# Kernel optimization log

Measured on AMD Instinct MI355X. Metric: run time of the kernel, lower is better.

Reference implementation:

```python
import jax, jax.numpy as jnp
import numpy as np

B, T, D, L, VOCAB = 4, 2048, 512, 3, 256


def setup_inputs() -> dict:
    key = jax.random.key(0)
    ks = jax.random.split(key, 5)
    x = jax.random.randint(ks[0], (B, T), 0, VOCAB, dtype=jnp.int32)
    embed = jax.random.normal(ks[1], (VOCAB, D), dtype=jnp.float32) * 0.02
    k = jnp.ones((L,), dtype=jnp.float32)
    ln_gamma = jnp.ones((L, D), dtype=jnp.float32)
    ln_beta = jnp.zeros((L, D), dtype=jnp.float32)
    W1 = jax.random.normal(ks[2], (L, D, 4 * D), dtype=jnp.float32) * 0.02
    b1 = jnp.zeros((L, 4 * D), dtype=jnp.float32)
    W2 = jax.random.normal(ks[3], (L, 4 * D, D), dtype=jnp.float32) * 0.02
    b2 = jnp.zeros((L, D), dtype=jnp.float32)
    return {"x": x, "embed": embed, "k": k, "ln_gamma": ln_gamma,
            "ln_beta": ln_beta, "W1": W1, "b1": b1, "W2": W2, "b2": b2}


def _layernorm(x, g, b, eps=1e-3):  # keras default eps=1e-3
    mu = jnp.mean(x, axis=-1, keepdims=True)
    var = jnp.mean(jnp.square(x - mu), axis=-1, keepdims=True)
    return (x - mu) * jax.lax.rsqrt(var + eps) * g + b


def reference(x, embed, k, ln_gamma, ln_beta, W1, b1, W2, b2):
    h = embed[x]  # (B,T,D)
    # CumprodBoundaryDimension: cumprod over feature dim, tanh, cumsum over time
    bd = jnp.cumsum(jnp.tanh(jnp.cumprod(h, axis=-1)), axis=1)
    h = h + h * bd
    t = jnp.arange(T)
    dist = jnp.abs((t[:, None] - t[None, :]).astype(jnp.float32))  # (T,T)
    causal = (t[None, :] <= t[:, None]).astype(jnp.float32)
    for l in range(L):
        # DeltaImportance
        h_cum = jnp.cumsum(h, axis=1)
        h_prev = jnp.pad(h[:, :-1, :], ((0, 0), (1, 0), (0, 0)))
        mag = jnp.linalg.norm(h_cum - h_prev, axis=-1)  # (B,T)
        decay = jnp.exp(-jax.nn.softplus(k[l]) * dist) * causal  # (T,T)
        # importance[b,i,j] = mag[b,i]*decay[i,j]; context = importance @ h
        ctx = jnp.abs(mag[:, :, None] * jnp.einsum('ij,bjd->bid', decay, h))
        y = _layernorm(ctx, ln_gamma[l], ln_beta[l])
        y = jax.nn.gelu(y @ W1[l] + b1[l], approximate=False) @ W2[l] + b2[l]
        h = h + y
    return h @ embed.T  # tied output projection (B,T,VOCAB)
```

## Files before the change

kernel.cpp:

```cpp
#include <hip/hip_runtime.h>
#include <math.h>


constexpr int Bc = 4, Tc = 2048, Dc = 512, Hc = 2048, Vc = 256;
constexpr int TSF = 16, NCF = 128;

typedef __attribute__((ext_vector_type(8))) short short8;
typedef __attribute__((ext_vector_type(4))) float f32x4;

__device__ inline unsigned short f2bf(float f) {
  unsigned int u = __float_as_uint(f);
  u += 0x7fffu + ((u >> 16) & 1u);
  return (unsigned short)(u >> 16);
}

__device__ inline void gload_lds16(const void* g, void* l) {
  __builtin_amdgcn_global_load_lds(
      (const __attribute__((address_space(1))) void*)g,
      (__attribute__((address_space(3))) void*)l, 16, 0, 0);
}

__device__ inline float gelu_f(float z) {
  float x = z * 0.707106781186547524f;
  float ax = fabsf(x);
  float t = 1.0f / (1.0f + 0.3275911f * ax);
  float poly = t*(0.254829592f + t*(-0.284496736f + t*(1.421413741f +
               t*(-1.453152027f + t*1.061405429f))));
  float er = 1.0f - poly * __expf(-ax*ax);
  er = copysignf(er, x);
  return 0.5f * z * (1.0f + er);
}

__device__ inline float decay_w(const float* kvec, int l) {
  float kk = kvec[l];
  float sp = kk > 0.f ? kk + log1pf(expf(-kk)) : log1pf(expf(kk));
  return expf(-sp);
}

__device__ inline void tr32(const float* Wl, unsigned short* Wtl,
                            int R, int C, int c0, int r0, int tid,
                            float (*tile)[33]) {
  int tx = tid & 31, ty = tid >> 5;
  for (int i = ty; i < 32; i += 8)
    tile[i][tx] = Wl[(size_t)(r0+i)*C + (c0+tx)];
  __syncthreads();
  int rx = tid & 7, ry = tid >> 3;
  ushort4 o;
  o.x = f2bf(tile[rx*4+0][ry]);
  o.y = f2bf(tile[rx*4+1][ry]);
  o.z = f2bf(tile[rx*4+2][ry]);
  o.w = f2bf(tile[rx*4+3][ry]);
  *(ushort4*)&Wtl[(size_t)(c0+ry)*R + (r0 + rx*4)] = o;
}

__global__ __launch_bounds__(256) void wprep(
    const float* __restrict__ W1, unsigned short* __restrict__ W1t,
    const float* __restrict__ W2, unsigned short* __restrict__ W2t,
    const float* __restrict__ embed, unsigned short* __restrict__ emb)
{
  __shared__ float tile[32][33];
  int bid = blockIdx.x, tid = threadIdx.x;
  if (bid < 3072) {
    int l = bid >> 10, rem = bid & 1023;
    int cx = rem & 63, ry = rem >> 6;
    tr32(W1 + (size_t)l*Dc*Hc, W1t + (size_t)l*Dc*Hc, Dc, Hc,
         cx*32, ry*32, tid, tile);
  } else if (bid < 6144) {
    int b2 = bid - 3072;
    int l = b2 >> 10, rem = b2 & 1023;
    int cx = rem & 15, ry = rem >> 4;
    tr32(W2 + (size_t)l*Hc*Dc, W2t + (size_t)l*Hc*Dc, Hc, Dc,
         cx*32, ry*32, tid, tile);
  } else {
    int i = ((bid - 6144)*256 + tid) * 4;
    if (i < Vc*Dc) {
      float4 v = *(const float4*)&embed[i];
      ushort4 o;
      o.x = f2bf(v.x); o.y = f2bf(v.y); o.z = f2bf(v.z); o.w = f2bf(v.w);
      *(ushort4*)&emb[i] = o;
    }
  }
}

__global__ __launch_bounds__(1024) void embed_part(
    const int* __restrict__ x, const float* __restrict__ embed,
    float* __restrict__ th, float* __restrict__ partA)
{
  int c = blockIdx.x, b = blockIdx.y;
  int wv = threadIdx.x >> 6, lane = threadIdx.x & 63;
  int token = b*Tc + c*TSF + wv;
  int row = x[token];
  const float* e = embed + (size_t)row * Dc + lane * 8;
  float v[8];
  {
    float4 a = *(const float4*)e;
    float4 bb = *(const float4*)(e + 4);
    v[0]=a.x; v[1]=a.y; v[2]=a.z; v[3]=a.w;
    v[4]=bb.x; v[5]=bb.y; v[6]=bb.z; v[7]=bb.w;
  }
  float p = v[0];
  #pragma unroll
  for (int j=1;j<8;++j) p *= v[j];
  float incl = p;
  #pragma unroll
  for (int off=1; off<64; off<<=1) {
    float t = __shfl_up(incl, off);
    if (lane >= off) incl *= t;
  }
  float excl = __shfl_up(incl, 1);
  if (lane == 0) excl = 1.0f;
  float cc = excl;
  float o[8];
  #pragma unroll
  for (int j=0;j<8;++j) { cc *= v[j]; o[j] = tanhf(cc); }
  float* dst = th + (size_t)token * Dc + lane * 8;
  *(float4*)dst     = make_float4(o[0],o[1],o[2],o[3]);
  *(float4*)(dst+4) = make_float4(o[4],o[5],o[6],o[7]);
  __syncthreads();
  int d = threadIdx.x;
  if (d < Dc) {
    const float* pp = th + ((size_t)b*Tc + c*TSF)*Dc + d;
    float s = 0.f;
    #pragma unroll
    for (int t=0;t<TSF;++t) s += pp[(size_t)t*Dc];
    partA[((size_t)b*NCF + c)*Dc + d] = s;
  }
}

__global__ __launch_bounds__(512) void part_prefix(float* __restrict__ part)
{
  int pair = blockIdx.x * 8 + (threadIdx.x >> 6);
  int lane = threadIdx.x & 63;
  int b = pair >> 9, d = pair & 511;
  size_t i0 = ((size_t)b*NCF + 2*lane)*Dc + d;
  float v0 = part[i0];
  float v1 = part[i0 + Dc];
  float ps = v0 + v1;
  float incl = ps;
  #pragma unroll
  for (int off=1; off<64; off<<=1) {
    float t = __shfl_up(incl, off);
    if (lane >= off) incl += t;
  }
  float excl = incl - ps;
  part[i0]      = excl;
  part[i0 + Dc] = excl + v0;
}

__global__ __launch_bounds__(512) void bd_apply(
    const float* __restrict__ th, const float* __restrict__ partA,
    const int* __restrict__ x, const float* __restrict__ embed,
    float* __restrict__ h, float* __restrict__ partB,
    float* __restrict__ partW, const float* __restrict__ kvec)
{
  int c = blockIdx.x, b = blockIdx.y, d = threadIdx.x;
  float w0 = decay_w(kvec, 0);
  float acc = partA[((size_t)b*NCF + c)*Dc + d];
  float hsum = 0.f, psW = 0.f;
  #pragma unroll
  for (int t=0;t<TSF;++t) {
    int tt = c*TSF + t;
    size_t idx = ((size_t)b*Tc + tt)*Dc + d;
    acc += th[idx];
    int row = x[b*Tc + tt];
    float e = embed[(size_t)row*Dc + d];
    float hv = e * (1.0f + acc);
    h[idx] = hv;
    hsum += hv;
    psW = psW * w0 + hv;
  }
  partB[((size_t)b*NCF + c)*Dc + d] = hsum;
  partW[((size_t)b*NCF + c)*Dc + d] = psW;
}

__global__ __launch_bounds__(512) void mag_scan_ln(
    const float* __restrict__ h, const float* __restrict__ part,
    const float* __restrict__ partW,
    const float* __restrict__ kvec, int l,
    const float* __restrict__ g, const float* __restrict__ bt,
    unsigned short* __restrict__ yb)
{
  __shared__ float redA[8][TSF];
  __shared__ float redB[8][TSF];
  __shared__ float mag[TSF], muS[TSF], rsS[TSF];
  int c = blockIdx.x, b = blockIdx.y, d = threadIdx.x;
  int lane = d & 63, wv = d >> 6;
  float acc = part[((size_t)b*NCF + c)*Dc + d];
  int t0 = c * TSF;
  const float* hbase = h + (size_t)b*Tc*Dc + d;
  float hp = (t0 > 0) ? hbase[(size_t)(t0-1)*Dc] : 0.f;
  float hv[TSF];
  #pragma unroll
  for (int t=0;t<TSF;++t) {
    hv[t] = hbase[(size_t)(t0+t)*Dc];
    acc += hv[t];
    float diff = acc - hp;
    hp = hv[t];
    float s = diff * diff;
    #pragma unroll
    for (int off=32; off; off>>=1) s += __shfl_down(s, off);
    if (!lane) redA[wv][t] = s;
  }
  float w = decay_w(kvec, l);
  float s = (c > 0) ? partW[((size_t)b*NCF + (c-1))*Dc + d] : 0.f;
  __syncthreads();
  if (d < TSF) {
    float m = 0.f;
    #pragma unroll
    for (int w2=0;w2<8;++w2) m += redA[w2][d];
    mag[d] = sqrtf(m);
  }
  __syncthreads();
  #pragma unroll
  for (int t=0;t<TSF;++t) {
    s = hv[t] + w * s;
    float cv = mag[t] * fabsf(s);
    hv[t] = cv;
    float s1 = cv, s2 = cv * cv;
    #pragma unroll
    for (int off=32; off; off>>=1) {
      s1 += __shfl_down(s1, off);
      s2 += __shfl_down(s2, off);
    }
    if (!lane) { redA[wv][t] = s1; redB[wv][t] = s2; }
  }
  __syncthreads();
  if (d < TSF) {
    float m1 = 0.f, m2 = 0.f;
    #pragma unroll
    for (int w2=0;w2<8;++w2) { m1 += redA[w2][d]; m2 += redB[w2][d]; }
    float mu = m1 * (1.f/Dc);
    float var = fmaxf(m2 * (1.f/Dc) - mu*mu, 0.f);
    muS[d] = mu;
    rsS[d] = rsqrtf(var + 1e-3f);
  }
  __syncthreads();
  float gv = g[l*Dc + d], bv = bt[l*Dc + d];
  unsigned short* yp = yb + ((size_t)b*Tc + t0)*Dc + d;
  #pragma unroll
  for (int t=0;t<TSF;++t)
    yp[(size_t)t*Dc] = f2bf((hv[t] - muS[t]) * rsS[t] * gv + bv);
}

template<int CH> __device__ inline int swz(int row) {
  if constexpr (CH == 8) return row & 7;
  else return (row & 3) ^ ((row >> 3) & 1);
}

template<int EPI, int TM, int TN, int BK>
__global__ __launch_bounds__(256) void mgemm(
    const unsigned short* __restrict__ A,
    const unsigned short* __restrict__ Bt,
    const float* __restrict__ bias,
    float* __restrict__ C, unsigned short* __restrict__ Cb,
    float* __restrict__ part, float* __restrict__ partW,
    const float* __restrict__ kvec, int wl,
    int N, int K, int nrow)
{
  constexpr int CH = BK / 8;
  constexpr int PA = TM*CH/256, PB = TN*CH/256;
  constexpr int WM = TM/2, WN = TN/2;
  constexpr int AM = WM/16, AN = WN/16;
  constexpr int NKH = BK/32;
  constexpr int ASTG = TM*BK, BSTG = TN*BK;
  __shared__ unsigned short As[2*ASTG];
  __shared__ unsigned short Bs[2*BSTG];
  int tid = threadIdx.x;
  int lane = tid & 63, w = tid >> 6;
  int wr = w >> 1, wc = w & 1;
  int bid = blockIdx.x;
  int xcd = bid & 7, i = bid >> 3;
  int npx = nrow >> 3;
  int m0 = (xcd * npx + (i % npx)) * TM;
  int n0 = (i / npx) * TN;

  const unsigned short* ag[PA];
  const unsigned short* bg[PB];
  int aldst[PA], bldst[PB];
  #pragma unroll
  for (int p=0;p<PA;++p) {
    int ci = p*256 + tid;
    int row = ci / CH, cp = ci % CH;
    int cg = cp ^ swz<CH>(row);
    ag[p] = A + (size_t)(m0+row)*K + cg*8;
    aldst[p] = (p*256 + w*64)*8;
  }
  #pragma unroll
  for (int p=0;p<PB;++p) {
    int ci = p*256 + tid;
    int row = ci / CH, cp = ci % CH;
    int cg = cp ^ swz<CH>(row);
    bg[p] = Bt + (size_t)(n0+row)*K + cg*8;
    bldst[p] = (p*256 + w*64)*8;
  }

  int r = lane & 15, quad = lane >> 4;
  int aoff[NKH][AM], boff[NKH][AN];
  #pragma unroll
  for (int kh=0;kh<NKH;++kh) {
    int cb = kh*4 + quad;
    #pragma unroll
    for (int i2=0;i2<AM;++i2)
      aoff[kh][i2] = (wr*WM + i2*16 + r)*BK + ((cb ^ swz<CH>(r)) & (CH-1))*8;
    #pragma unroll
    for (int j=0;j<AN;++j)
      boff[kh][j] = (wc*WN + j*16 + r)*BK + ((cb ^ swz<CH>(r)) & (CH-1))*8;
  }

  f32x4 acc[AM][AN];
  #pragma unroll
  for (int i2=0;i2<AM;++i2)
    #pragma unroll
    for (int j=0;j<AN;++j)
      acc[i2][j] = (f32x4){0.f,0.f,0.f,0.f};

  #pragma unroll
  for (int p=0;p<PA;++p) gload_lds16(ag[p], &As[aldst[p]]);
  #pragma unroll
  for (int p=0;p<PB;++p) gload_lds16(bg[p], &Bs[bldst[p]]);

  int nk = K / BK;
  for (int ki = 0; ki < nk; ++ki) {
    __syncthreads();
    int cur = ki & 1, nxt = cur ^ 1;
    if (ki + 1 < nk) {
      int kk = (ki + 1) * BK;
      #pragma unroll
      for (int p=0;p<PA;++p) gload_lds16(ag[p] + kk, &As[nxt*ASTG + aldst[p]]);
      #pragma unroll
      for (int p=0;p<PB;++p) gload_lds16(bg[p] + kk, &Bs[nxt*BSTG + bldst[p]]);
    }
    #pragma unroll
    for (int kh=0;kh<NKH;++kh) {
      short8 af[AM], bfr[AN];
      #pragma unroll
      for (int i2=0;i2<AM;++i2) af[i2] = *(const short8*)&As[cur*ASTG + aoff[kh][i2]];
      #pragma unroll
      for (int j=0;j<AN;++j) bfr[j] = *(const short8*)&Bs[cur*BSTG + boff[kh][j]];
      #pragma unroll
      for (int i2=0;i2<AM;++i2)
        #pragma unroll
        for (int j=0;j<AN;++j)
          acc[i2][j] = __builtin_amdgcn_mfma_f32_16x16x32_bf16(af[i2], bfr[j], acc[i2][j], 0, 0, 0);
    }
  }

  float wnext = 0.f, invw = 0.f, pwbase = 0.f;
  if (EPI == 1 && partW) {
    wnext = decay_w(kvec, wl);
    invw = 1.0f / wnext;
    pwbase = 1.0f;
    for (int q = 0; q < 15 - quad*4; ++q) pwbase *= wnext;
  }

  #pragma unroll
  for (int i2=0;i2<AM;++i2) {
    int rowb = m0 + wr*WM + i2*16 + quad*4;
    #pragma unroll
    for (int j=0;j<AN;++j) {
      int col = n0 + wc*WN + j*16 + r;
      float bv = 0.f;
      if (EPI != 2) bv = bias[col];
      float ps = 0.f, psW = 0.f, pw = pwbase;
      #pragma unroll
      for (int reg=0;reg<4;++reg) {
        size_t idx = (size_t)(rowb + reg) * N + col;
        float z = acc[i2][j][reg] + bv;
        if (EPI == 0) {
          Cb[idx] = f2bf(gelu_f(z));
        } else if (EPI == 1) {
          float hv = C[idx] + z;
          C[idx] = hv;
          ps += hv;
          if (partW) { psW += pw * hv; pw *= invw; }
          if (Cb) Cb[idx] = f2bf(hv);
        } else {
          C[idx] = z;
        }
      }
      if (EPI == 1 && part) {
        ps += __shfl_xor(ps, 16);
        ps += __shfl_xor(ps, 32);
        if (partW) {
          psW += __shfl_xor(psW, 16);
          psW += __shfl_xor(psW, 32);
        }
        if (quad == 0) {
          int chunk = (m0 + wr*WM + i2*16) >> 4;
          part[(size_t)chunk * N + col] = ps;
          if (partW) partW[(size_t)chunk * N + col] = psW;
        }
      }
    }
  }
}

extern "C" void kernel_launch(void* const* d_in, const int* in_sizes, int n_in,
                              void* d_out, int out_size, void* d_ws, size_t ws_size,
                              hipStream_t stream) {
  const int*   x     = (const int*)  d_in[0];
  const float* embed = (const float*)d_in[1];
  const float* kvec  = (const float*)d_in[2];
  const float* g     = (const float*)d_in[3];
  const float* bt    = (const float*)d_in[4];
  const float* W1    = (const float*)d_in[5];
  const float* b1    = (const float*)d_in[6];
  const float* W2    = (const float*)d_in[7];
  const float* b2    = (const float*)d_in[8];
  float* out = (float*)d_out;

  const size_t NTD = (size_t)Bc * Tc * Dc;
  const size_t NTH = (size_t)Bc * Tc * Hc;
  char* wsb = (char*)d_ws;
  float* h      = (float*)wsb;                wsb += NTD*4;
  float* tmpA   = (float*)wsb;                wsb += NTD*4;
  float* partA  = (float*)wsb;                wsb += (size_t)Bc*NCF*Dc*4;
  float* partB  = (float*)wsb;                wsb += (size_t)Bc*NCF*Dc*4;
  float* partW  = (float*)wsb;                wsb += (size_t)Bc*NCF*Dc*4;
  unsigned short* yb   = (unsigned short*)wsb; wsb += NTD*2;
  unsigned short* a1b  = (unsigned short*)wsb; wsb += NTH*2;
  unsigned short* hb   = (unsigned short*)wsb; wsb += NTD*2;
  unsigned short* W1t  = (unsigned short*)wsb; wsb += (size_t)3*Dc*Hc*2;
  unsigned short* W2t  = (unsigned short*)wsb; wsb += (size_t)3*Dc*Hc*2;
  unsigned short* emb  = (unsigned short*)wsb; wsb += (size_t)Vc*Dc*2;

  wprep<<<dim3(6144 + (Vc*Dc)/1024), 256, 0, stream>>>(
      W1, W1t, W2, W2t, embed, emb);

  embed_part<<<dim3(NCF, Bc), 1024, 0, stream>>>(x, embed, tmpA, partA);
  part_prefix<<<dim3(256), 512, 0, stream>>>(partA);
  bd_apply<<<dim3(NCF, Bc), 512, 0, stream>>>(tmpA, partA, x, embed, h,
                                              partB, partW, kvec);
  part_prefix<<<dim3(256), 512, 0, stream>>>(partB);

  for (int l = 0; l < 3; ++l) {
    mag_scan_ln<<<dim3(NCF, Bc), 512, 0, stream>>>(h, partB, partW, kvec, l,
                                                   g, bt, yb);
    mgemm<0,128,128,32><<<dim3(64*(Hc/128)), 256, 0, stream>>>(
        yb, W1t + (size_t)l*Hc*Dc, b1 + (size_t)l*Hc, nullptr, a1b,
        nullptr, nullptr, kvec, 0, Hc, Dc, 64);
    mgemm<1,128,64,64><<<dim3(64*(Dc/64)), 256, 0, stream>>>(
        a1b, W2t + (size_t)l*Dc*Hc, b2 + (size_t)l*Dc, h,
        (l == 2) ? hb : nullptr,
        (l < 2) ? partB : nullptr, (l < 2) ? partW : nullptr, kvec, l + 1,
        Dc, Hc, 64);
    if (l < 2) part_prefix<<<dim3(256), 512, 0, stream>>>(partB);
  }
  mgemm<2,64,64,32><<<dim3(128*(Vc/64)), 256, 0, stream>>>(
      hb, emb, nullptr, out, nullptr, nullptr, nullptr, kvec, 0,
      Vc, Dc, 128);
}
```

Before: 424.5 us.

## Deepen GEMM pipeline to four LDS stages with explicit vmcnt waits

Replaces the double-buffered global-to-LDS load loop in the MFMA GEMM with a four-slot ring that keeps three tiles in flight, using explicit s_waitcnt vmcnt counts and a raw s_barrier instead of __syncthreads. The aim is to hide global load latency better. It also changes the LDS swizzle for BK=32 tiles, cuts the W2 GEMM's BK from 64 to 32 so the larger ring fits in LDS, and uses a fast reciprocal in GELU. The larger LDS footprint may lower occupancy, and the hand-written waitcnt logic risks races if the counts do not match the outstanding loads.

```diff
diff --git a/kernel.cpp b/kernel.cpp
--- a/kernel.cpp
+++ b/kernel.cpp
@@ -20,10 +20,23 @@
       (__attribute__((address_space(3))) void*)l, 16, 0, 0);
 }
 
+template<int N> __device__ inline void wvm() {
+  if constexpr (N == 0)      asm volatile("s_waitcnt vmcnt(0)" ::: "memory");
+  else if constexpr (N == 2) asm volatile("s_waitcnt vmcnt(2)" ::: "memory");
+  else if constexpr (N == 3) asm volatile("s_waitcnt vmcnt(3)" ::: "memory");
+  else if constexpr (N == 4) asm volatile("s_waitcnt vmcnt(4)" ::: "memory");
+  else if constexpr (N == 6) asm volatile("s_waitcnt vmcnt(6)" ::: "memory");
+  else if constexpr (N == 8) asm volatile("s_waitcnt vmcnt(8)" ::: "memory");
+  else static_assert(N == 0, "unsupported vmcnt");
+}
+__device__ inline void barrier_raw() {
+  asm volatile("s_barrier" ::: "memory");
+}
+
 __device__ inline float gelu_f(float z) {
   float x = z * 0.707106781186547524f;
   float ax = fabsf(x);
-  float t = 1.0f / (1.0f + 0.3275911f * ax);
+  float t = __builtin_amdgcn_rcpf(fmaf(0.3275911f, ax, 1.0f));
   float poly = t*(0.254829592f + t*(-0.284496736f + t*(1.421413741f +
                t*(-1.453152027f + t*1.061405429f))));
   float er = 1.0f - poly * __expf(-ax*ax);
@@ -244,7 +257,7 @@
 
 template<int CH> __device__ inline int swz(int row) {
   if constexpr (CH == 8) return row & 7;
-  else return (row & 3) ^ ((row >> 3) & 1);
+  else return (row >> 1) & 3;
 }
 
 template<int EPI, int TM, int TN, int BK>
@@ -259,12 +272,13 @@
 {
   constexpr int CH = BK / 8;
   constexpr int PA = TM*CH/256, PB = TN*CH/256;
+  constexpr int LPT = PA + PB;
   constexpr int WM = TM/2, WN = TN/2;
   constexpr int AM = WM/16, AN = WN/16;
   constexpr int NKH = BK/32;
   constexpr int ASTG = TM*BK, BSTG = TN*BK;
-  __shared__ unsigned short As[2*ASTG];
-  __shared__ unsigned short Bs[2*BSTG];
+  __shared__ unsigned short As[4*ASTG];
+  __shared__ unsigned short Bs[4*BSTG];
   int tid = threadIdx.x;
   int lane = tid & 63, w = tid >> 6;
   int wr = w >> 1, wc = w & 1;
@@ -314,22 +328,25 @@
     for (int j=0;j<AN;++j)
       acc[i2][j] = (f32x4){0.f,0.f,0.f,0.f};
 
-  #pragma unroll
-  for (int p=0;p<PA;++p) gload_lds16(ag[p], &As[aldst[p]]);
-  #pragma unroll
-  for (int p=0;p<PB;++p) gload_lds16(bg[p], &Bs[bldst[p]]);
+  auto STAGE = [&](int t) {
+    int kk = t * BK;
+    int sl = t & 3;
+    #pragma unroll
+    for (int p=0;p<PA;++p) gload_lds16(ag[p] + kk, &As[sl*ASTG + aldst[p]]);
+    #pragma unroll
+    for (int p=0;p<PB;++p) gload_lds16(bg[p] + kk, &Bs[sl*BSTG + bldst[p]]);
+  };
 
   int nk = K / BK;
+  STAGE(0); STAGE(1); STAGE(2);
+
   for (int ki = 0; ki < nk; ++ki) {
-    __syncthreads();
-    int cur = ki & 1, nxt = cur ^ 1;
-    if (ki + 1 < nk) {
-      int kk = (ki + 1) * BK;
-      #pragma unroll
-      for (int p=0;p<PA;++p) gload_lds16(ag[p] + kk, &As[nxt*ASTG + aldst[p]]);
-      #pragma unroll
-      for (int p=0;p<PB;++p) gload_lds16(bg[p] + kk, &Bs[nxt*BSTG + bldst[p]]);
-    }
+    if (ki < nk-2)       wvm<2*LPT>();
+    else if (ki == nk-2) wvm<LPT>();
+    else                 wvm<0>();
+    barrier_raw();
+    if (ki + 3 < nk) STAGE(ki + 3);
+    int cur = ki & 3;
     #pragma unroll
     for (int kh=0;kh<NKH;++kh) {
       short8 af[AM], bfr[AN];
@@ -439,7 +456,7 @@
     mgemm<0,128,128,32><<<dim3(64*(Hc/128)), 256, 0, stream>>>(
         yb, W1t + (size_t)l*Hc*Dc, b1 + (size_t)l*Hc, nullptr, a1b,
         nullptr, nullptr, kvec, 0, Hc, Dc, 64);
-    mgemm<1,128,64,64><<<dim3(64*(Dc/64)), 256, 0, stream>>>(
+    mgemm<1,128,64,32><<<dim3(64*(Dc/64)), 256, 0, stream>>>(
         a1b, W2t + (size_t)l*Dc*Hc, b2 + (size_t)l*Dc, h,
         (l == 2) ? hb : nullptr,
         (l < 2) ? partB : nullptr, (l < 2) ? partW : nullptr, kvec, l + 1,
```

Measured after the change: 428.1 us. Within noise of the previous version (+0.8%).

## Add 256x256 four-stage pipelined bf16 MFMA GEMM for the W1 projection

Applied to the files above, without the earlier changes.

Replaces the 128x128 GEMM used for the first MLP projection with a dedicated 512-thread kernel. It uses 256x256 tiles, a 4-deep LDS ring filled by direct global-to-LDS loads, explicit vmcnt waits with raw barriers, and MFMA bursts raised with setprio, with the GELU epilogue fused in. The goal is fewer blocks, more reuse per loaded tile and better overlap of loads with MFMA work. It also switches GELU's divide to a hardware reciprocal and changes the BK=32 LDS swizzle pattern, which the other GEMM instances also use. The raw waitcnt and barrier choreography is fragile, and with one large block per CU, occupancy and tail behaviour are at risk.

```diff
diff --git a/kernel.cpp b/kernel.cpp
--- a/kernel.cpp
+++ b/kernel.cpp
@@ -20,10 +20,20 @@
       (__attribute__((address_space(3))) void*)l, 16, 0, 0);
 }
 
+template<int N> __device__ inline void wvm() {
+  if constexpr (N == 0)      asm volatile("s_waitcnt vmcnt(0)" ::: "memory");
+  else if constexpr (N == 4) asm volatile("s_waitcnt vmcnt(4)" ::: "memory");
+  else if constexpr (N == 8) asm volatile("s_waitcnt vmcnt(8)" ::: "memory");
+  else static_assert(N == 0, "unsupported vmcnt");
+}
+__device__ inline void barrier_raw() {
+  asm volatile("s_barrier" ::: "memory");
+}
+
 __device__ inline float gelu_f(float z) {
   float x = z * 0.707106781186547524f;
   float ax = fabsf(x);
-  float t = 1.0f / (1.0f + 0.3275911f * ax);
+  float t = __builtin_amdgcn_rcpf(fmaf(0.3275911f, ax, 1.0f));
   float poly = t*(0.254829592f + t*(-0.284496736f + t*(1.421413741f +
                t*(-1.453152027f + t*1.061405429f))));
   float er = 1.0f - poly * __expf(-ax*ax);
@@ -244,7 +254,131 @@
 
 template<int CH> __device__ inline int swz(int row) {
   if constexpr (CH == 8) return row & 7;
-  else return (row & 3) ^ ((row >> 3) & 1);
+  else return (row >> 1) & 3;
+}
+
+__global__ __launch_bounds__(512, 2) void mgemm8(
+    const unsigned short* __restrict__ A,
+    const unsigned short* __restrict__ Bt,
+    const float* __restrict__ bias,
+    unsigned short* __restrict__ Cb,
+    int N, int K, int nrow)
+{
+  constexpr int TM = 256, TN = 256, BK = 32;
+  constexpr int PA = 2, PB = 2;
+  constexpr int ASTG = TM*BK, BSTG = TN*BK;
+  __shared__ unsigned short As[4*ASTG];
+  __shared__ unsigned short Bs[4*BSTG];
+  int tid = threadIdx.x;
+  int lane = tid & 63, w = tid >> 6;
+  int wr = w >> 2, wc = w & 3;
+  int bid = blockIdx.x;
+  int xcd = bid & 7, i = bid >> 3;
+  int npx = nrow >> 3;
+  int m0 = (xcd * npx + (i % npx)) * TM;
+  int n0 = (i / npx) * TN;
+
+  const unsigned short* ag[PA];
+  const unsigned short* bg[PB];
+  int aldst[PA], bldst[PB];
+  #pragma unroll
+  for (int p=0;p<PA;++p) {
+    int ci = p*512 + tid;
+    int row = ci >> 2, cp = ci & 3;
+    int cg = cp ^ ((row >> 1) & 3);
+    ag[p] = A + (size_t)(m0+row)*K + cg*8;
+    aldst[p] = (p*512 + w*64)*8;
+  }
+  #pragma unroll
+  for (int p=0;p<PB;++p) {
+    int ci = p*512 + tid;
+    int row = ci >> 2, cp = ci & 3;
+    int cg = cp ^ ((row >> 1) & 3);
+    bg[p] = Bt + (size_t)(n0+row)*K + cg*8;
+    bldst[p] = (p*512 + w*64)*8;
+  }
+
+  int r = lane & 15, quad = lane >> 4;
+  int sz = (quad ^ ((r >> 1) & 3)) * 8;
+  int aoff[8], boff[4];
+  #pragma unroll
+  for (int fi=0; fi<8; ++fi)
+    aoff[fi] = (wr*128 + fi*16 + r)*BK + sz;
+  #pragma unroll
+  for (int fj=0; fj<4; ++fj)
+    boff[fj] = (wc*64 + fj*16 + r)*BK + sz;
+
+  f32x4 acc[8][4];
+  #pragma unroll
+  for (int fi=0;fi<8;++fi)
+    #pragma unroll
+    for (int fj=0;fj<4;++fj)
+      acc[fi][fj] = (f32x4){0.f,0.f,0.f,0.f};
+
+  auto STAGE_A = [&](int t) {
+    int kk = t * BK, sl = t & 3;
+    #pragma unroll
+    for (int p=0;p<PA;++p) gload_lds16(ag[p] + kk, &As[sl*ASTG + aldst[p]]);
+  };
+  auto STAGE_B = [&](int t) {
+    int kk = t * BK, sl = t & 3;
+    #pragma unroll
+    for (int p=0;p<PB;++p) gload_lds16(bg[p] + kk, &Bs[sl*BSTG + bldst[p]]);
+  };
+
+  int nk = K / BK;
+  STAGE_A(0); STAGE_B(0);
+  STAGE_A(1); STAGE_B(1);
+  STAGE_A(2); STAGE_B(2);
+
+  for (int kt = 0; kt < nk; ++kt) {
+    if (kt < nk-2)       wvm<8>();
+    else if (kt == nk-2) wvm<4>();
+    else                 wvm<0>();
+    barrier_raw();
+    int s = kt & 3;
+    short8 bfr[4], af[4];
+    #pragma unroll
+    for (int fj=0;fj<4;++fj) bfr[fj] = *(const short8*)&Bs[s*BSTG + boff[fj]];
+    #pragma unroll
+    for (int fi=0;fi<4;++fi) af[fi] = *(const short8*)&As[s*ASTG + aoff[fi]];
+    if (kt + 3 < nk) STAGE_A(kt + 3);
+    __builtin_amdgcn_s_setprio(1);
+    #pragma unroll
+    for (int fi=0;fi<4;++fi)
+      #pragma unroll
+      for (int fj=0;fj<4;++fj)
+        acc[fi][fj] = __builtin_amdgcn_mfma_f32_16x16x32_bf16(
+            af[fi], bfr[fj], acc[fi][fj], 0, 0, 0);
+    __builtin_amdgcn_s_setprio(0);
+    barrier_raw();
+    #pragma unroll
+    for (int fi=0;fi<4;++fi) af[fi] = *(const short8*)&As[s*ASTG + aoff[4+fi]];
+    if (kt + 3 < nk) STAGE_B(kt + 3);
+    __builtin_amdgcn_s_setprio(1);
+    #pragma unroll
+    for (int fi=0;fi<4;++fi)
+      #pragma unroll
+      for (int fj=0;fj<4;++fj)
+        acc[4+fi][fj] = __builtin_amdgcn_mfma_f32_16x16x32_bf16(
+            af[fi], bfr[fj], acc[4+fi][fj], 0, 0, 0);
+    __builtin_amdgcn_s_setprio(0);
+  }
+
+  #pragma unroll
+  for (int fi=0;fi<8;++fi) {
+    int rowb = m0 + wr*128 + fi*16 + quad*4;
+    #pragma unroll
+    for (int fj=0;fj<4;++fj) {
+      int col = n0 + wc*64 + fj*16 + r;
+      float bv = bias[col];
+      #pragma unroll
+      for (int reg=0;reg<4;++reg) {
+        size_t idx = (size_t)(rowb + reg) * N + col;
+        Cb[idx] = f2bf(gelu_f(acc[fi][fj][reg] + bv));
+      }
+    }
+  }
 }
 
 template<int EPI, int TM, int TN, int BK>
@@ -366,9 +500,7 @@
       for (int reg=0;reg<4;++reg) {
         size_t idx = (size_t)(rowb + reg) * N + col;
         float z = acc[i2][j][reg] + bv;
-        if (EPI == 0) {
-          Cb[idx] = f2bf(gelu_f(z));
-        } else if (EPI == 1) {
+        if (EPI == 1) {
           float hv = C[idx] + z;
           C[idx] = hv;
           ps += hv;
@@ -436,9 +568,8 @@
   for (int l = 0; l < 3; ++l) {
     mag_scan_ln<<<dim3(NCF, Bc), 512, 0, stream>>>(h, partB, partW, kvec, l,
                                                    g, bt, yb);
-    mgemm<0,128,128,32><<<dim3(64*(Hc/128)), 256, 0, stream>>>(
-        yb, W1t + (size_t)l*Hc*Dc, b1 + (size_t)l*Hc, nullptr, a1b,
-        nullptr, nullptr, kvec, 0, Hc, Dc, 64);
+    mgemm8<<<dim3(256), 512, 0, stream>>>(
+        yb, W1t + (size_t)l*Hc*Dc, b1 + (size_t)l*Hc, a1b, Hc, Dc, 32);
     mgemm<1,128,64,64><<<dim3(64*(Dc/64)), 256, 0, stream>>>(
         a1b, W2t + (size_t)l*Dc*Hc, b2 + (size_t)l*Dc, h,
         (l == 2) ? hb : nullptr,
```

Measured after the change: 392.7 us. -7.5%, faster.
